# Performance work log

Hardware: AMD Instinct MI355X
Metric: run time of the kernel (lower is better)

The kernel has to match this reference:

```python
import jax, jax.numpy as jnp
import numpy as np

B, T, H = 64, 1024, 256

def _lstm_cell(x, h, c, Wih, Whh, bih, bhh):
    # torch gate order: i, f, g, o
    gates = x @ Wih.T + h @ Whh.T + bih + bhh  # [B, 4H]
    i, f, g, o = jnp.split(gates, 4, axis=-1)
    i = jax.nn.sigmoid(i)
    f = jax.nn.sigmoid(f)
    g = jnp.tanh(g)
    o = jax.nn.sigmoid(o)
    c_new = f * c + i * g
    h_new = o * jnp.tanh(c_new)
    return h_new, c_new


def setup_inputs() -> dict:
    key = jax.random.key(0)
    ks = jax.random.split(key, 11)
    s = 1.0 / np.sqrt(H)
    def u(k, shape):
        return jax.random.uniform(k, shape, jnp.float32, -s, s)
    return {
        "x": jax.random.normal(ks[0], (B, T, 1), jnp.float32),
        "enc_Wih": u(ks[1], (4 * H, 1)),
        "enc_Whh": u(ks[2], (4 * H, H)),
        "enc_bih": u(ks[3], (4 * H,)),
        "enc_bhh": u(ks[4], (4 * H,)),
        "dec_Wih": u(ks[5], (4 * H, 1)),
        "dec_Whh": u(ks[6], (4 * H, H)),
        "dec_bih": u(ks[7], (4 * H,)),
        "dec_bhh": u(ks[8], (4 * H,)),
        "lin_W": u(ks[9], (1, 2 * H)),
        "lin_b": u(ks[10], (1,)),
    }


def reference(x, enc_Wih, enc_Whh, enc_bih, enc_bhh,
              dec_Wih, dec_Whh, dec_bih, dec_bhh, lin_W, lin_b):
    b = x.shape[0]
    h = x.shape[2] * 0  # placeholder, not used
    hidden = enc_Whh.shape[1]

    x_t = jnp.transpose(x, (1, 0, 2))  # [T, B, 1]

    # ---- encoder: single-layer LSTM over time ----
    def enc_step(carry, xt):
        hh, cc = carry
        hh, cc = _lstm_cell(xt, hh, cc, enc_Wih, enc_Whh, enc_bih, enc_bhh)
        return (hh, cc), hh
    h0 = jnp.zeros((b, hidden), x.dtype)
    (h_last, _), enc_seq = jax.lax.scan(enc_step, (h0, h0), x_t)
    encoder_states = jnp.transpose(enc_seq, (1, 0, 2))  # [B, T, H]

    # ---- decoder: LSTMCell + dot attention + linear, per step ----
    def dec_step(carry, xt):
        hx, cx = carry
        hx, cx = _lstm_cell(xt, hx, cx, dec_Wih, dec_Whh, dec_bih, dec_bhh)
        scores = jnp.einsum('bth,bh->bt', encoder_states, hx)  # dot attention
        attn = jax.nn.softmax(scores, axis=1)
        ctx = jnp.einsum('bt,bth->bh', attn, encoder_states)
        updated = jnp.concatenate([ctx, hx], axis=1)  # [B, 2H]
        res = updated @ lin_W.T + lin_b  # [B, 1]
        return (hx, cx), res

    cx0 = jnp.zeros_like(h_last)
    _, outs = jax.lax.scan(dec_step, (h_last, cx0), x_t)  # [T, B, 1]
    return jnp.transpose(outs, (1, 0, 2))  # [B, T, 1]
```

## Files before the change

### kernel.cpp

```cpp
#include <hip/hip_runtime.h>
#include <math.h>

#define HD 256
#define GD 1024
#define TT 1024
#define BB 64
#define NT 512

__device__ __forceinline__ float sig_(float x)  { return 1.f / (1.f + __expf(-x)); }
__device__ __forceinline__ float tanh_(float x) { return 1.f - 2.f / (1.f + __expf(2.f * x)); }

__global__ __launch_bounds__(256) void prep_kernel(
    const float* __restrict__ eW, const float* __restrict__ eb1, const float* __restrict__ eb2,
    const float* __restrict__ dW, const float* __restrict__ db1, const float* __restrict__ db2,
    float* __restrict__ WTe, float* __restrict__ WTd,
    float* __restrict__ be, float* __restrict__ bd,
    unsigned long long* __restrict__ ex_all)
{
    int idx = blockIdx.x * 256 + threadIdx.x;
    if (idx < GD * HD) {
        int j = idx / HD, k = idx % HD;
        WTe[k * GD + j] = eW[idx];
        WTd[k * GD + j] = dW[idx];
    }
    if (idx < GD) {
        be[idx] = eb1[idx] + eb2[idx];
        bd[idx] = db1[idx] + db2[idx];
    }
    if (idx < 2 * BB * 2 * 256) ex_all[idx] = 0ULL;
}

__global__ __launch_bounds__(NT, 2) void lstm_scan_coop(
    const float* __restrict__ x,
    const float* __restrict__ Wih,
    const float* __restrict__ bias,
    const float* __restrict__ WT,
    const float* __restrict__ h_init,
    float* __restrict__ states,
    unsigned long long* __restrict__ ex)
{
    const int b   = blockIdx.x & 63;
    const int q   = blockIdx.x >> 6;
    const int tid = threadIdx.x;
    const int s   = tid & 3;
    const int jj  = tid >> 2;
    const int gate = jj >> 5;
    const int kk0  = (jj & 31) * 2;
    const int r0   = gate * 64 + kk0;
    const int jg0  = gate * 256 + q * 64 + kk0;

    __shared__ float h_rep[4][264];
    __shared__ float act_s[256];
    __shared__ float x_s[TT];

    float4 w0[16], w1[16];
    {
        const float* basek = WT + (size_t)(s * 64) * GD;
        #pragma unroll
        for (int i = 0; i < 16; ++i) {
            const float* p0 = basek + (size_t)(4 * i) * GD + jg0;
            w0[i] = make_float4(p0[0], p0[GD], p0[2 * GD], p0[3 * GD]);
            const float* p1 = p0 + 1;
            w1[i] = make_float4(p1[0], p1[GD], p1[2 * GD], p1[3 * GD]);
        }
    }
    const float wih0 = Wih[jg0], wih1 = Wih[jg0 + 1];
    const float bj0  = bias[jg0], bj1  = bias[jg0 + 1];

    for (int i = tid; i < TT; i += NT) x_s[i] = x[b * TT + i];
    if (tid < 256) {
        float hv = h_init ? h_init[((size_t)b * TT + (TT - 1)) * HD + tid] : 0.f;
        h_rep[tid >> 6][tid & 63] = hv;
    }
    float c = 0.f;
    __syncthreads();

    for (int t = 0; t < TT; ++t) {
        const float xt = x_s[t];
        float a0p, a1p, a0q = 0.f, a1q = 0.f;
        if (s == 0) { a0p = fmaf(xt, wih0, bj0); a1p = fmaf(xt, wih1, bj1); }
        else        { a0p = 0.f;                 a1p = 0.f; }
        const float4* h4 = (const float4*)(&h_rep[s][0]);
        #pragma unroll
        for (int i = 0; i < 8; ++i) {
            float4 hv = h4[i];
            a0p = fmaf(hv.x, w0[i].x, a0p); a0p = fmaf(hv.y, w0[i].y, a0p);
            a0p = fmaf(hv.z, w0[i].z, a0p); a0p = fmaf(hv.w, w0[i].w, a0p);
            a1p = fmaf(hv.x, w1[i].x, a1p); a1p = fmaf(hv.y, w1[i].y, a1p);
            a1p = fmaf(hv.z, w1[i].z, a1p); a1p = fmaf(hv.w, w1[i].w, a1p);
        }
        #pragma unroll
        for (int i = 8; i < 16; ++i) {
            float4 hv = h4[i];
            a0q = fmaf(hv.x, w0[i].x, a0q); a0q = fmaf(hv.y, w0[i].y, a0q);
            a0q = fmaf(hv.z, w0[i].z, a0q); a0q = fmaf(hv.w, w0[i].w, a0q);
            a1q = fmaf(hv.x, w1[i].x, a1q); a1q = fmaf(hv.y, w1[i].y, a1q);
            a1q = fmaf(hv.z, w1[i].z, a1q); a1q = fmaf(hv.w, w1[i].w, a1q);
        }
        float a0 = a0p + a0q;
        float a1 = a1p + a1q;
        a0 += __shfl_xor(a0, 1); a0 += __shfl_xor(a0, 2);
        a1 += __shfl_xor(a1, 1); a1 += __shfl_xor(a1, 2);
        if (s == 0) {
            float2 av;
            av.x = (gate == 2) ? tanh_(a0) : sig_(a0);
            av.y = (gate == 2) ? tanh_(a1) : sig_(a1);
            *(float2*)(&act_s[r0]) = av;
        }
        __syncthreads();

        unsigned long long* slot = ex + ((size_t)b * 2 + (t & 1)) * 256;
        if (tid < 256) {
            const int dq = tid >> 6, dk = tid & 63;
            if (dq == q) {
                float gi = act_s[dk], gf = act_s[64 + dk], gg = act_s[128 + dk], go = act_s[192 + dk];
                c = fmaf(gf, c, gi * gg);
                float h = go * tanh_(c);
                unsigned long long pk = ((unsigned long long)(unsigned)(t + 1) << 32)
                                      | (unsigned long long)__float_as_uint(h);
                __hip_atomic_store(&slot[tid], pk, __ATOMIC_RELAXED, __HIP_MEMORY_SCOPE_AGENT);
                h_rep[q][dk] = h;
                states[((size_t)(b * TT + t)) * HD + tid] = h;
            } else {
                unsigned long long u;
                do {
                    u = __hip_atomic_load(&slot[tid], __ATOMIC_RELAXED, __HIP_MEMORY_SCOPE_AGENT);
                } while ((unsigned)(u >> 32) != (unsigned)(t + 1));
                h_rep[dq][dk] = __uint_as_float((unsigned)u);
            }
        }
        __syncthreads();
    }
}

__global__ __launch_bounds__(256) void proj_kernel(
    const float* __restrict__ enc_states, const float* __restrict__ dec_hs,
    const float* __restrict__ linW, float* __restrict__ ew, float* __restrict__ hw)
{
    const int lane = threadIdx.x & 63;
    const int wid  = blockIdx.x * 4 + (threadIdx.x >> 6);
    const int nw   = gridDim.x * 4;
    const float4 w1 = ((const float4*)linW)[lane];
    const float4 w2 = ((const float4*)(linW + HD))[lane];
    for (int o = wid; o < BB * TT; o += nw) {
        float4 v1 = ((const float4*)(enc_states + (size_t)o * HD))[lane];
        float4 v2 = ((const float4*)(dec_hs     + (size_t)o * HD))[lane];
        float s1 = v1.x * w1.x + v1.y * w1.y + v1.z * w1.z + v1.w * w1.w;
        float s2 = v2.x * w2.x + v2.y * w2.y + v2.z * w2.z + v2.w * w2.w;
        #pragma unroll
        for (int m = 1; m < 64; m <<= 1) {
            s1 += __shfl_xor(s1, m);
            s2 += __shfl_xor(s2, m);
        }
        if (lane == 0) { ew[o] = s1; hw[o] = s2; }
    }
}

#define TD2  32
#define TEC2 256
#define KC2  32
__global__ __launch_bounds__(256) void attn_kernel(
    const float* __restrict__ enc_states,
    const float* __restrict__ dec_hs,
    const float* __restrict__ ew, const float* __restrict__ hw,
    const float* __restrict__ lin_b,
    float* __restrict__ out)
{
    const int b   = blockIdx.y;
    const int td0 = blockIdx.x * TD2;
    const int tid = threadIdx.x;
    const int tdt = tid >> 5;
    const int tet = tid & 31;

    __shared__ float Hx[HD][TD2 + 4];
    __shared__ float E[KC2][TEC2];

    {
        const int td = tid >> 3;
        const int kc = (tid & 7) * 32;
        const float* src = dec_hs + ((size_t)b * TT + td0 + td) * HD + kc;
        #pragma unroll
        for (int qq = 0; qq < 8; ++qq) {
            float4 v = ((const float4*)(src + qq * 4))[0];
            Hx[kc + qq * 4 + 0][td] = v.x;
            Hx[kc + qq * 4 + 1][td] = v.y;
            Hx[kc + qq * 4 + 2][td] = v.z;
            Hx[kc + qq * 4 + 3][td] = v.w;
        }
    }

    float M[4]  = {-1e30f, -1e30f, -1e30f, -1e30f};
    float Nm[4] = {0.f, 0.f, 0.f, 0.f};
    float Dn[4] = {0.f, 0.f, 0.f, 0.f};

    for (int tc = 0; tc < TT / TEC2; ++tc) {
        const int te0 = tc * TEC2;
        float S[4][8] = {{0.f}};
        for (int kc = 0; kc < HD / KC2; ++kc) {
            const int k0 = kc * KC2;
            __syncthreads();
            {
                const float* src = enc_states + ((size_t)b * TT + te0 + tid) * HD + k0;
                #pragma unroll
                for (int qq = 0; qq < 8; ++qq) {
                    float4 v = ((const float4*)(src + qq * 4))[0];
                    E[qq * 4 + 0][tid] = v.x;
                    E[qq * 4 + 1][tid] = v.y;
                    E[qq * 4 + 2][tid] = v.z;
                    E[qq * 4 + 3][tid] = v.w;
                }
            }
            __syncthreads();
            #pragma unroll 4
            for (int k = 0; k < KC2; ++k) {
                const float4 hx4 = *(const float4*)(&Hx[k0 + k][tdt * 4]);
                #pragma unroll
                for (int i = 0; i < 8; ++i) {
                    const float e = E[k][tet + 32 * i];
                    S[0][i] = fmaf(hx4.x, e, S[0][i]);
                    S[1][i] = fmaf(hx4.y, e, S[1][i]);
                    S[2][i] = fmaf(hx4.z, e, S[2][i]);
                    S[3][i] = fmaf(hx4.w, e, S[3][i]);
                }
            }
        }
        float ewv[8];
        #pragma unroll
        for (int i = 0; i < 8; ++i) ewv[i] = ew[(size_t)b * TT + te0 + tet + 32 * i];
        #pragma unroll
        for (int r = 0; r < 4; ++r) {
            float cm = S[r][0];
            #pragma unroll
            for (int i = 1; i < 8; ++i) cm = fmaxf(cm, S[r][i]);
            #pragma unroll
            for (int m = 1; m < 32; m <<= 1) cm = fmaxf(cm, __shfl_xor(cm, m));
            const float newM  = fmaxf(M[r], cm);
            const float scale = __expf(M[r] - newM);
            float nl = 0.f, dl = 0.f;
            #pragma unroll
            for (int i = 0; i < 8; ++i) {
                const float p = __expf(S[r][i] - newM);
                dl += p;
                nl = fmaf(p, ewv[i], nl);
            }
            #pragma unroll
            for (int m = 1; m < 32; m <<= 1) {
                nl += __shfl_xor(nl, m);
                dl += __shfl_xor(dl, m);
            }
            Nm[r] = Nm[r] * scale + nl;
            Dn[r] = Dn[r] * scale + dl;
            M[r]  = newM;
        }
    }

    if (tet == 0) {
        const float lb = lin_b[0];
        #pragma unroll
        for (int r = 0; r < 4; ++r) {
            const int td = td0 + tdt * 4 + r;
            out[(size_t)b * TT + td] = Nm[r] / Dn[r] + hw[(size_t)b * TT + td] + lb;
        }
    }
}

extern "C" void kernel_launch(void* const* d_in, const int* in_sizes, int n_in,
                              void* d_out, int out_size, void* d_ws, size_t ws_size,
                              hipStream_t stream)
{
    const float* x    = (const float*)d_in[0];
    const float* eWih = (const float*)d_in[1];
    const float* eWhh = (const float*)d_in[2];
    const float* ebih = (const float*)d_in[3];
    const float* ebhh = (const float*)d_in[4];
    const float* dWih = (const float*)d_in[5];
    const float* dWhh = (const float*)d_in[6];
    const float* dbih = (const float*)d_in[7];
    const float* dbhh = (const float*)d_in[8];
    const float* linW = (const float*)d_in[9];
    const float* linb = (const float*)d_in[10];
    float* out = (float*)d_out;

    float* p = (float*)d_ws;
    float* WTe = p;        p += (size_t)GD * HD;
    float* WTd = p;        p += (size_t)GD * HD;
    float* be  = p;        p += GD;
    float* bd  = p;        p += GD;
    float* enc_states = p; p += (size_t)BB * TT * HD;
    float* dec_hs = p;     p += (size_t)BB * TT * HD;
    float* ew = p;         p += (size_t)BB * TT;
    float* hw = p;         p += (size_t)BB * TT;
    unsigned long long* ex_e = (unsigned long long*)p; p += (size_t)BB * 2 * 256 * 2;
    unsigned long long* ex_d = (unsigned long long*)p; p += (size_t)BB * 2 * 256 * 2;

    prep_kernel<<<(GD * HD + 255) / 256, 256, 0, stream>>>(
        eWhh, ebih, ebhh, dWhh, dbih, dbhh, WTe, WTd, be, bd, ex_e);

    {
        const float* hi = nullptr;
        void* args[] = {(void*)&x, (void*)&eWih, (void*)&be, (void*)&WTe,
                        (void*)&hi, (void*)&enc_states, (void*)&ex_e};
        hipLaunchCooperativeKernel((void*)lstm_scan_coop, dim3(256), dim3(NT),
                                   args, 0, stream);
    }
    {
        const float* hi = enc_states;
        void* args[] = {(void*)&x, (void*)&dWih, (void*)&bd, (void*)&WTd,
                        (void*)&hi, (void*)&dec_hs, (void*)&ex_d};
        hipLaunchCooperativeKernel((void*)lstm_scan_coop, dim3(256), dim3(NT),
                                   args, 0, stream);
    }

    proj_kernel<<<256, 256, 0, stream>>>(enc_states, dec_hs, linW, ew, hw);
    attn_kernel<<<dim3(TT / TD2, BB), 256, 0, stream>>>(enc_states, dec_hs, ew, hw, linb, out);
}
```

Before: 3.943 ms.

## Remove per-step block barrier by exchanging gates via wave shuffles

The thread mapping is reorganised so that all four gates for a hidden unit sit in the same wavefront. Gate activations are exchanged with cross-lane shuffles rather than through shared memory plus a __syncthreads, and every wave computes the cell update redundantly. The writes of h to the exchange slots, the local shared copy and the global states are spread across different lane groups. The encoder and decoder now share one exchange buffer, kept distinct by a tag offset, and are launched as normal kernels instead of cooperative launches. The cost is duplicated cell math, plus a reliance on all 256 blocks being co-resident without the cooperative-launch guarantee.

```diff
diff --git a/kernel.cpp b/kernel.cpp
--- a/kernel.cpp
+++ b/kernel.cpp
@@ -15,7 +15,7 @@
     const float* __restrict__ dW, const float* __restrict__ db1, const float* __restrict__ db2,
     float* __restrict__ WTe, float* __restrict__ WTd,
     float* __restrict__ be, float* __restrict__ bd,
-    unsigned long long* __restrict__ ex_all)
+    unsigned long long* __restrict__ ex)
 {
     int idx = blockIdx.x * 256 + threadIdx.x;
     if (idx < GD * HD) {
@@ -27,30 +27,31 @@
         be[idx] = eb1[idx] + eb2[idx];
         bd[idx] = db1[idx] + db2[idx];
     }
-    if (idx < 2 * BB * 2 * 256) ex_all[idx] = 0ULL;
-}
-
-__global__ __launch_bounds__(NT, 2) void lstm_scan_coop(
+    if (idx < BB * 2 * 256) ex[idx] = 0ULL;
+}
+
+__global__ __launch_bounds__(NT, 2) void lstm_scan(
     const float* __restrict__ x,
     const float* __restrict__ Wih,
     const float* __restrict__ bias,
     const float* __restrict__ WT,
     const float* __restrict__ h_init,
     float* __restrict__ states,
-    unsigned long long* __restrict__ ex)
-{
-    const int b   = blockIdx.x & 63;
-    const int q   = blockIdx.x >> 6;
-    const int tid = threadIdx.x;
-    const int s   = tid & 3;
-    const int jj  = tid >> 2;
-    const int gate = jj >> 5;
-    const int kk0  = (jj & 31) * 2;
-    const int r0   = gate * 64 + kk0;
-    const int jg0  = gate * 256 + q * 64 + kk0;
+    unsigned long long* __restrict__ ex,
+    unsigned tag0)
+{
+    const int b    = (int)blockIdx.x & 63;
+    const int q    = (int)blockIdx.x >> 6;
+    const int tid  = threadIdx.x;
+    const int lane = tid & 63;
+    const int wv   = tid >> 6;
+    const int g    = lane >> 4;
+    const int s    = (lane >> 2) & 3;
+    const int dl   = lane & 3;
+    const int d    = wv * 4 + dl;
+    const int jg0  = g * 256 + q * 64 + 2 * d;
 
     __shared__ float h_rep[4][264];
-    __shared__ float act_s[256];
     __shared__ float x_s[TT];
 
     float4 w0[16], w1[16];
@@ -72,7 +73,7 @@
         float hv = h_init ? h_init[((size_t)b * TT + (TT - 1)) * HD + tid] : 0.f;
         h_rep[tid >> 6][tid & 63] = hv;
     }
-    float c = 0.f;
+    float c0 = 0.f, c1 = 0.f;
     __syncthreads();
 
     for (int t = 0; t < TT; ++t) {
@@ -99,33 +100,50 @@
         }
         float a0 = a0p + a0q;
         float a1 = a1p + a1q;
-        a0 += __shfl_xor(a0, 1); a0 += __shfl_xor(a0, 2);
-        a1 += __shfl_xor(a1, 1); a1 += __shfl_xor(a1, 2);
+        a0 += __shfl_xor(a0, 4); a0 += __shfl_xor(a0, 8);
+        a1 += __shfl_xor(a1, 4); a1 += __shfl_xor(a1, 8);
+        float av0 = (g == 2) ? tanh_(a0) : sig_(a0);
+        float av1 = (g == 2) ? tanh_(a1) : sig_(a1);
+        float p16_0 = __shfl_xor(av0, 16), p32_0 = __shfl_xor(av0, 32);
+        float p48_0 = __shfl_xor(p32_0, 16);
+        float p16_1 = __shfl_xor(av1, 16), p32_1 = __shfl_xor(av1, 32);
+        float p48_1 = __shfl_xor(p32_1, 16);
+        float gi0, gf0, gg0, go0, gi1, gf1, gg1, go1;
+        if      (g == 0) { gi0=av0;   gf0=p16_0; gg0=p32_0; go0=p48_0;
+                           gi1=av1;   gf1=p16_1; gg1=p32_1; go1=p48_1; }
+        else if (g == 1) { gi0=p16_0; gf0=av0;   gg0=p48_0; go0=p32_0;
+                           gi1=p16_1; gf1=av1;   gg1=p48_1; go1=p32_1; }
+        else if (g == 2) { gi0=p32_0; gf0=p48_0; gg0=av0;   go0=p16_0;
+                           gi1=p32_1; gf1=p48_1; gg1=av1;   go1=p16_1; }
+        else             { gi0=p48_0; gf0=p32_0; gg0=p16_0; go0=av0;
+                           gi1=p48_1; gf1=p32_1; gg1=p16_1; go1=av1; }
+        c0 = fmaf(gf0, c0, gi0 * gg0);
+        c1 = fmaf(gf1, c1, gi1 * gg1);
+        const float h0 = go0 * tanh_(c0);
+        const float h1 = go1 * tanh_(c1);
+
+        const unsigned tag = tag0 + (unsigned)t + 1u;
+        unsigned long long* ssl = ex + ((size_t)b * 2 + (t & 1)) * 256;
         if (s == 0) {
-            float2 av;
-            av.x = (gate == 2) ? tanh_(a0) : sig_(a0);
-            av.y = (gate == 2) ? tanh_(a1) : sig_(a1);
-            *(float2*)(&act_s[r0]) = av;
-        }
-        __syncthreads();
-
-        unsigned long long* slot = ex + ((size_t)b * 2 + (t & 1)) * 256;
+            if (g < 2) {
+                unsigned long long pk = ((unsigned long long)tag << 32)
+                    | (unsigned long long)__float_as_uint(g == 0 ? h0 : h1);
+                __hip_atomic_store(&ssl[q * 64 + 2 * d + g], pk,
+                                   __ATOMIC_RELAXED, __HIP_MEMORY_SCOPE_AGENT);
+            } else if (g == 2) {
+                *(float2*)(&h_rep[q][2 * d]) = make_float2(h0, h1);
+            } else {
+                *(float2*)(&states[((size_t)(b * TT + t)) * HD + q * 64 + 2 * d])
+                    = make_float2(h0, h1);
+            }
+        }
         if (tid < 256) {
             const int dq = tid >> 6, dk = tid & 63;
-            if (dq == q) {
-                float gi = act_s[dk], gf = act_s[64 + dk], gg = act_s[128 + dk], go = act_s[192 + dk];
-                c = fmaf(gf, c, gi * gg);
-                float h = go * tanh_(c);
-                unsigned long long pk = ((unsigned long long)(unsigned)(t + 1) << 32)
-                                      | (unsigned long long)__float_as_uint(h);
-                __hip_atomic_store(&slot[tid], pk, __ATOMIC_RELAXED, __HIP_MEMORY_SCOPE_AGENT);
-                h_rep[q][dk] = h;
-                states[((size_t)(b * TT + t)) * HD + tid] = h;
-            } else {
+            if (dq != q) {
                 unsigned long long u;
                 do {
-                    u = __hip_atomic_load(&slot[tid], __ATOMIC_RELAXED, __HIP_MEMORY_SCOPE_AGENT);
-                } while ((unsigned)(u >> 32) != (unsigned)(t + 1));
+                    u = __hip_atomic_load(&ssl[tid], __ATOMIC_RELAXED, __HIP_MEMORY_SCOPE_AGENT);
+                } while ((unsigned)(u >> 32) != tag);
                 h_rep[dq][dk] = __uint_as_float((unsigned)u);
             }
         }
@@ -290,26 +308,15 @@
     float* dec_hs = p;     p += (size_t)BB * TT * HD;
     float* ew = p;         p += (size_t)BB * TT;
     float* hw = p;         p += (size_t)BB * TT;
-    unsigned long long* ex_e = (unsigned long long*)p; p += (size_t)BB * 2 * 256 * 2;
-    unsigned long long* ex_d = (unsigned long long*)p; p += (size_t)BB * 2 * 256 * 2;
+    unsigned long long* ex = (unsigned long long*)p; p += (size_t)BB * 2 * 256 * 2;
 
     prep_kernel<<<(GD * HD + 255) / 256, 256, 0, stream>>>(
-        eWhh, ebih, ebhh, dWhh, dbih, dbhh, WTe, WTd, be, bd, ex_e);
-
-    {
-        const float* hi = nullptr;
-        void* args[] = {(void*)&x, (void*)&eWih, (void*)&be, (void*)&WTe,
-                        (void*)&hi, (void*)&enc_states, (void*)&ex_e};
-        hipLaunchCooperativeKernel((void*)lstm_scan_coop, dim3(256), dim3(NT),
-                                   args, 0, stream);
-    }
-    {
-        const float* hi = enc_states;
-        void* args[] = {(void*)&x, (void*)&dWih, (void*)&bd, (void*)&WTd,
-                        (void*)&hi, (void*)&dec_hs, (void*)&ex_d};
-        hipLaunchCooperativeKernel((void*)lstm_scan_coop, dim3(256), dim3(NT),
-                                   args, 0, stream);
-    }
+        eWhh, ebih, ebhh, dWhh, dbih, dbhh, WTe, WTd, be, bd, ex);
+
+    lstm_scan<<<256, NT, 0, stream>>>(
+        x, eWih, be, WTe, nullptr, enc_states, ex, 0u);
+    lstm_scan<<<256, NT, 0, stream>>>(
+        x, dWih, bd, WTd, enc_states, dec_hs, ex, 1024u);
 
     proj_kernel<<<256, 256, 0, stream>>>(enc_states, dec_hs, linW, ew, hw);
     attn_kernel<<<dim3(TT / TD2, BB), 256, 0, stream>>>(enc_states, dec_hs, ew, hw, linb, out);
```

Result: slower. 4.983 ms (+26.4%).
